# Performance work log

Hardware: AMD Instinct MI355X
Metric: run time of the kernel (lower is better)

The kernel has to match this reference:

```python
import jax, jax.numpy as jnp
import numpy as np

B, N, C, D, K, H, A = 4, 2048, 128, 128, 16, 64, 512


def _rn(k, shape, s):
    return (jax.random.normal(k, shape) * s).astype(jnp.float32)


def setup_inputs():
    ks = jax.random.split(jax.random.key(0), 40)
    w = lambda i, o, c: _rn(ks[i], (o, c), 0.02)
    b = lambda i, o: _rn(ks[i + 20], (o,), 0.02)
    p = {}
    p["xyz"] = _rn(ks[0], (B, 3, N), 1.0)
    p["pos"] = _rn(ks[1], (B, 2, N), 1.0)
    p["key"] = _rn(ks[2], (B, C, N), 1.0)
    p["query"] = _rn(ks[3], (B, C, N), 1.0)
    p["mv_w1"] = w(4, C, 2 * C); p["mv_b1"] = b(4, C)
    p["mv_w2"] = w(5, C, C);     p["mv_b2"] = b(5, C)
    p["mv_ws"] = w(6, C, 2 * C); p["mv_bs"] = b(6, C)
    p["wk"] = w(7, D, C); p["bk"] = b(7, D)
    p["wq"] = w(8, D, C); p["bq"] = b(8, D)
    p["wv"] = w(9, D, C); p["bv"] = b(9, D)
    p["xyz_w1"] = w(10, H, 3); p["xyz_b1"] = b(10, H)
    p["xyz_w2"] = w(11, D, H); p["xyz_b2"] = b(11, D)
    p["pos_w1"] = w(12, H, 2); p["pos_b1"] = b(12, H)
    p["pos_w2"] = w(13, D, H); p["pos_b2"] = b(13, D)
    p["xat_w1"] = w(14, A, D); p["xat_b1"] = b(14, A)
    p["xat_w2"] = w(15, D, A); p["xat_b2"] = b(15, D)
    p["at_w1"] = w(16, A, D); p["at_b1"] = b(16, A)
    p["at_w2"] = w(17, D, A); p["at_b2"] = b(17, D)
    p["wkq"] = w(18, C, D); p["bkq"] = b(18, C)
    p["wend"] = w(19, C, D); p["bend"] = b(19, C)
    return p


def c1(w, b, x):  # 1x1 Conv1d: (O,C) on (B,C,N)
    return jnp.einsum('oc,bcn->bon', w, x) + b[None, :, None]


def c2(w, b, x):  # 1x1 Conv2d: (O,C) on (B,C,N,K)
    return jnp.einsum('oc,bcnk->bonk', w, x) + b[None, :, None, None]


def mlp2(w1, b1, w2, b2, x):
    return c2(w2, b2, jax.nn.relu(c2(w1, b1, x)))


def softmax_one(x):  # exp(x-m) / (1 + sum exp(x-m)) over last axis
    m = jnp.max(x, axis=-1, keepdims=True)
    e = jnp.exp(x - m)
    return e / (1.0 + jnp.sum(e, axis=-1, keepdims=True))


def knn_idx(pts, k):  # pts: (B, N, d) -> (B, N, k) indices, include_self=True
    sq = jnp.sum(pts * pts, axis=-1)
    d2 = sq[:, :, None] + sq[:, None, :] - 2.0 * jnp.einsum('bnd,bmd->bnm', pts, pts)
    return jnp.argsort(d2, axis=-1)[:, :, :k]


def group(f, idx):  # f: (B,C,N), idx: (B,N,K) -> (B,C,N,K)
    return jax.vmap(lambda a, i: a[:, i])(f, idx)


def reference(xyz, pos, key, query, mv_w1, mv_b1, mv_w2, mv_b2, mv_ws, mv_bs,
              wk, bk, wq, bq, wv, bv, xyz_w1, xyz_b1, xyz_w2, xyz_b2,
              pos_w1, pos_b1, pos_w2, pos_b2, xat_w1, xat_b1, xat_w2, xat_b2,
              at_w1, at_b1, at_w2, at_b2, wkq, bkq, wend, bend):
    cat = jnp.concatenate([key, query], axis=1)  # (B, 2C, N)
    # MLP_Res
    value = c1(mv_w2, mv_b2, jax.nn.relu(c1(mv_w1, mv_b1, cat))) + c1(mv_ws, mv_bs, cat)
    identity = value
    k = c1(wk, bk, key)
    q = c1(wq, bq, query)
    v = c1(wv, bv, value)
    # ---- block 1: xyz-space kNN attention ----
    idx1 = knn_idx(jnp.swapaxes(xyz, 1, 2), K)           # (B,N,K)
    kq_rel = k[..., None] - group(q, idx1)               # (B,D,N,K)
    xyz_rel = xyz[..., None] - group(xyz, idx1)          # (B,3,N,K)
    xyz_emb = mlp2(xyz_w1, xyz_b1, xyz_w2, xyz_b2, xyz_rel)
    xa = softmax_one(mlp2(xat_w1, xat_b1, xat_w2, xat_b2, kq_rel + xyz_emb))
    agg = jnp.sum(xa * (v[..., None] + xyz_emb), axis=-1)  # (B,D,N)
    value = c1(wkq, bkq, agg) + identity
    value = c1(wv, bv, value)
    # ---- block 2: pos-space kNN attention ----
    idx2 = knn_idx(jnp.swapaxes(pos, 1, 2), K)
    qk_rel = q[..., None] - group(k, idx2)
    pos_rel = pos[..., None] - group(pos, idx2)
    pos_emb = mlp2(pos_w1, pos_b1, pos_w2, pos_b2, pos_rel)
    at = softmax_one(mlp2(at_w1, at_b1, at_w2, at_b2, qk_rel + pos_emb))
    agg = jnp.sum(at * (value[..., None] + pos_emb), axis=-1)
    y = c1(wend, bend, agg)
    return y + identity
```

## Files before the change

kernel.cpp:

```cpp
#include <hip/hip_runtime.h>
#include <hip/hip_bf16.h>

typedef __hip_bfloat16 bf16;
typedef unsigned long long ull;

#define BB 4
#define NN 2048
#define CCH 128
#define DDM 128
#define KNB 16
#define HHD 64
#define AAD 512
#define PP (BB*NN)

typedef __attribute__((ext_vector_type(8))) short short8;
typedef __attribute__((ext_vector_type(16))) float f32x16;

__device__ __forceinline__ float b2f(bf16 x) { return __bfloat162float(x); }
__device__ __forceinline__ bf16 f2b(float x) { return __float2bfloat16(x); }

__device__ __forceinline__ float ldany(const void* p, size_t i, int f32) {
  return f32 ? ((const float*)p)[i] : __bfloat162float(((const bf16*)p)[i]);
}

__device__ __forceinline__ long pack4(float a, float b, float c, float d) {
  union { bf16 h[4]; long l; } u;
  u.h[0] = f2b(a); u.h[1] = f2b(b); u.h[2] = f2b(c); u.h[3] = f2b(d);
  return u.l;
}
__device__ __forceinline__ void unpack4(long l, float* o) {
  union { bf16 h[4]; long l; } u; u.l = l;
  o[0] = b2f(u.h[0]); o[1] = b2f(u.h[1]); o[2] = b2f(u.h[2]); o[3] = b2f(u.h[3]);
}

__device__ __forceinline__ short8 ldfrag(const bf16* base, int row, int stride, int k0, int hl) {
  const bf16* p = base + (size_t)row * stride + k0 + (hl << 3);
  union { short8 v; long l[2]; } u;
  u.l[0] = *(const long*)p;
  u.l[1] = *(const long*)(p + 4);
  return u.v;
}

__device__ __forceinline__ f32x16 MFMA(short8 a, short8 b, f32x16 c) {
  return __builtin_amdgcn_mfma_f32_32x32x16_bf16(a, b, c, 0, 0, 0);
}

struct PtrArr { const void* p[36]; int n[36]; };
struct CvtTab { int src[16]; int off[16]; int n[16]; int isb[16]; };
struct G4 { const bf16* X[4]; int K[4]; int woff[4]; int boff[4]; bf16* out[4]; int relu[4]; };

__global__ __launch_bounds__(256) void sniff_kern(PtrArr pa, int* __restrict__ flags) {
  int t = blockIdx.x;
  const bf16* x = (const bf16*)pa.p[t];
  int n = pa.n[t]; if (n > 4096) n = 4096;
  __shared__ int cnt;
  if (threadIdx.x == 0) cnt = 0;
  __syncthreads();
  int c = 0;
  for (int i = threadIdx.x; i < n; i += 256) {
    float v = fabsf(__bfloat162float(x[i]));
    if (v == 0.f || (v >= 1e-6f && v <= 1024.f)) c++;
  }
  atomicAdd(&cnt, c);
  __syncthreads();
  if (threadIdx.x == 0) flags[t] = (cnt >= (n * 7) / 8) ? 0 : 1;
}

__global__ __launch_bounds__(256) void cvtprep_kern(PtrArr pa, CvtTab tab,
                                                    const int* __restrict__ flags,
                                                    bf16* __restrict__ warena, float* __restrict__ barena,
                                                    bf16* __restrict__ w1img0, bf16* __restrict__ w2img0,
                                                    bf16* __restrict__ cw2img0, float* __restrict__ fb0,
                                                    bf16* __restrict__ w1img1, bf16* __restrict__ w2img1,
                                                    bf16* __restrict__ cw2img1, float* __restrict__ fb1) {
  int y = blockIdx.y;
  if (y >= 2) {
    int e = y - 2;
    int i = blockIdx.x * 256 + threadIdx.x;
    if (i >= tab.n[e]) return;
    float v = ldany(pa.p[tab.src[e]], i, flags[tab.src[e]]);
    if (tab.isb[e]) barena[tab.off[e] + i] = v;
    else warena[tab.off[e] + i] = f2b(v);
    return;
  }
  int set = y;
  int cIdx = set ? 20 : 16, aIdx = set ? 28 : 24, dd = set ? 2 : 3;
  bf16* w1img = set ? w1img1 : w1img0;
  bf16* w2img = set ? w2img1 : w2img0;
  bf16* cw2img = set ? cw2img1 : cw2img0;
  float* fb = set ? fb1 : fb0;
  const void* cw1 = pa.p[cIdx];     const void* cb1 = pa.p[cIdx + 1];
  const void* cw2 = pa.p[cIdx + 2]; const void* cb2 = pa.p[cIdx + 3];
  const void* aw1 = pa.p[aIdx];     const void* ab1 = pa.p[aIdx + 1];
  const void* aw2 = pa.p[aIdx + 2]; const void* ab2 = pa.p[aIdx + 3];
  int i = blockIdx.x * 256 + threadIdx.x;
  const int fcw1 = flags[cIdx], fcb1 = flags[cIdx + 1];
  const int fcw2 = flags[cIdx + 2], fcb2 = flags[cIdx + 3];
  const int faw1 = flags[aIdx], fab1 = flags[aIdx + 1];
  const int faw2 = flags[aIdx + 2], fab2 = flags[aIdx + 3];
  float* ab1f = fb;
  float* ab2f = fb + 512;
  float* cb1f = fb + 640;
  float* cb2f = fb + 704;
  float* cw1f = fb + 832;
  if (i < 65536) {
    int hg = i >> 7, c = i & 127;
    w1img[(size_t)hg * 132 + c] = f2b(ldany(aw1, i, faw1));
  } else if (i < 131072) {
    int j = i - 65536;
    int o = j >> 9, hh = j & 511;
    int ac = hh >> 7, hloc = hh & 127;
    w2img[(size_t)(ac * 128 + o) * 132 + hloc] = f2b(ldany(aw2, j, faw2));
  } else if (i < 139264) {
    int j = i - 131072;
    int o = j >> 6, h = j & 63;
    cw2img[o * 68 + h] = f2b(ldany(cw2, j, fcw2));
  } else if (i < 139776) {
    int j = i - 139264; ab1f[j] = ldany(ab1, j, fab1);
  } else if (i < 139904) {
    int j = i - 139776; ab2f[j] = ldany(ab2, j, fab2);
  } else if (i < 139968) {
    int j = i - 139904; cb1f[j] = ldany(cb1, j, fcb1);
  } else if (i < 140096) {
    int j = i - 139968; cb2f[j] = ldany(cb2, j, fcb2);
  } else if (i < 140288) {
    int j = i - 140096;
    int h = j / 3, c = j % 3;
    cw1f[j] = (c < dd) ? ldany(cw1, h * dd + c, fcw1) : 0.f;
  }
}

__global__ __launch_bounds__(256) void trall_kern(const void* __restrict__ keyp,
                                                  const void* __restrict__ qryp,
                                                  const void* __restrict__ xyzp,
                                                  const void* __restrict__ posp,
                                                  const int* __restrict__ flags,
                                                  bf16* __restrict__ catT,
                                                  float* __restrict__ xyzT,
                                                  float* __restrict__ posT,
                                                  bf16* __restrict__ warena,
                                                  float* __restrict__ barena) {
  int bx = blockIdx.x;
  int tid = threadIdx.x;
  if (bx < 512) {
    __shared__ float tile[64][65];
    int xx = bx & 31, yy = (bx >> 5) & 1, zz = bx >> 6;
    int b = zz & 3, half = zz >> 2;
    const void* src = half ? qryp : keyp;
    const int f32 = flags[2 + half];
    int n0 = xx * 64, c0 = yy * 64;
    int tx = tid & 63, ty = tid >> 6;
    for (int r = ty; r < 64; r += 4)
      tile[r][tx] = ldany(src, (size_t)(b * 128 + c0 + r) * NN + n0 + tx, f32);
    __syncthreads();
    for (int r = ty; r < 64; r += 4)
      catT[(size_t)(b * NN + n0 + r) * 256 + half * 128 + c0 + tx] = __float2bfloat16(tile[tx][r]);
    return;
  }
  if (bx < 768) {
    int cb = bx - 512;
    int which = cb >> 7;
    const void* src = which ? posp : xyzp;
    float* dst = which ? posT : xyzT;
    int dd = which ? 2 : 3;
    const int f32 = flags[which];
    int i = (cb & 127) * 256 * 2 + tid;
    for (int rep = 0; rep < 2; ++rep, i += 256) {
      if (i < PP * 4) {
        int p = i >> 2, j = i & 3;
        int b = p >> 11, n = p & (NN - 1);
        dst[i] = (j < dd) ? ldany(src, (size_t)(b * dd + j) * NN + n, f32) : 0.f;
      }
    }
    return;
  }
  int bx2 = bx - 768;
  const bf16* wv = warena + 114688;
  const bf16* wkq = warena + 131072;
  if (bx2 < 64) {
    int i = bx2 * 256 + tid;
    int row = i >> 7, col = i & 127;
    float acc = 0.f;
    for (int k = 0; k < 128; ++k)
      acc += b2f(wv[row * 128 + k]) * b2f(wkq[k * 128 + col]);
    warena[163840 + i] = f2b(acc);
  } else if (tid < 128) {
    float acc = 0.f;
    const float* bkq = barena + 768;
    for (int k = 0; k < 128; ++k)
      acc += b2f(wv[tid * 128 + k]) * bkq[k];
    barena[1024 + tid] = acc;
  }
}

__global__ __launch_bounds__(512) void mega_kern(
    const float* __restrict__ xyzT, const float* __restrict__ posT,
    int* __restrict__ idx1, int* __restrict__ idx2,
    G4 g, const bf16* __restrict__ warena, const float* __restrict__ barena) {
  __shared__ __attribute__((aligned(16))) char smem[33280];
  int bx = blockIdx.x;
  int tid = threadIdx.x, lane = tid & 63, wvv = tid >> 6;
  if (bx < 2048) {
    float4* cds = (float4*)smem;
    int set = bx >> 10;
    int pblk = bx & 1023;
    const float* coordsT = set ? posT : xyzT;
    int* idxout = set ? idx2 : idx1;
    int p0 = pblk * 8, b = p0 >> 11;
    for (int j = tid; j < NN; j += 512)
      cds[j] = *(const float4*)&coordsT[((size_t)(b << 11) + j) * 4];
    __syncthreads();
    int p = p0 + wvv, n = p & (NN - 1);
    float4 cc = cds[n];
    float sqi = __fadd_rn(__fadd_rn(__fmul_rn(cc.x, cc.x), __fmul_rn(cc.y, cc.y)),
                          __fmul_rn(cc.z, cc.z));
    ull t[32];
#pragma unroll
    for (int s = 0; s < 32; ++s) {
      int j = (s << 6) | lane;
      float4 q = cds[j];
      float sqj = __fadd_rn(__fadd_rn(__fmul_rn(q.x, q.x), __fmul_rn(q.y, q.y)),
                            __fmul_rn(q.z, q.z));
      float dt  = __fadd_rn(__fadd_rn(__fmul_rn(cc.x, q.x), __fmul_rn(cc.y, q.y)),
                            __fmul_rn(cc.z, q.z));
      float d2 = __fsub_rn(__fadd_rn(sqi, sqj), __fmul_rn(2.f, dt));
      unsigned u = __float_as_uint(d2);
      u = (u & 0x80000000u) ? ~u : (u | 0x80000000u);
      t[s] = ((ull)u << 32) | (unsigned)j;
    }
#pragma unroll
    for (int base = 0; base < 32; base += 16) {
#pragma unroll
      for (int k = 2; k <= 16; k <<= 1) {
#pragma unroll
        for (int j = k >> 1; j > 0; j >>= 1) {
#pragma unroll
          for (int i = 0; i < 16; ++i) {
            int l = i ^ j;
            if (l > i) {
              bool up = ((i & k) == 0);
              ull a = t[base + i], c = t[base + l];
              ull lo = a < c ? a : c;
              ull hi = a < c ? c : a;
              t[base + i] = up ? lo : hi;
              t[base + l] = up ? hi : lo;
            }
          }
        }
      }
    }
#pragma unroll
    for (int i = 0; i < 16; ++i) {
      ull a = t[i], c = t[31 - i];
      t[i] = a < c ? a : c;
    }
#pragma unroll
    for (int j = 8; j > 0; j >>= 1) {
#pragma unroll
      for (int i = 0; i < 16; ++i) {
        int l = i ^ j;
        if (l > i) {
          ull a = t[i], c = t[l];
          ull lo = a < c ? a : c;
          ull hi = a < c ? c : a;
          t[i] = lo; t[l] = hi;
        }
      }
    }
    for (int r = 0; r < KNB; ++r) {
      ull h = t[0];
      ull m = h;
#pragma unroll
      for (int off = 1; off < 64; off <<= 1) {
        ull o = __shfl_xor(m, off);
        m = o < m ? o : m;
      }
      if (lane == 0) idxout[(size_t)p * KNB + r] = (int)(m & 0xffffffffu);
      if (h == m) {
#pragma unroll
        for (int i = 0; i < 15; ++i) t[i] = t[i + 1];
        t[15] = ~0ull;
      }
    }
    return;
  }
  {
    bf16* XT = (bf16*)smem;
    int bx2 = bx - 2048;
    int op = bx2 >> 7, ptile = bx2 & 127;
    const bf16* X = g.X[op];
    int K = g.K[op];
    const bf16* Wb = warena + g.woff[op];
    const float* bias = barena + g.boff[op];
    bf16* out = g.out[op];
    int relu = g.relu[op];
    int hl = lane >> 5, cA = lane & 31;
    int p0 = ptile * 64;
    int SK = K + 4;
    int kc = K >> 3;
    for (int c = tid; c < 64 * kc; c += 512) {
      int r = c / kc, col = (c % kc) << 3;
      *(float4*)&XT[r * SK + col] = *(const float4*)&X[(size_t)(p0 + r) * 256 + col];
    }
    __syncthreads();
    int o0 = (wvv & 3) * 32;
    int tt = wvv >> 2;
    f32x16 acc;
#pragma unroll
    for (int r = 0; r < 16; ++r) {
      int o = o0 + (r & 3) + 8 * (r >> 2) + 4 * hl;
      acc[r] = bias[o];
    }
    for (int ks = 0; ks < (K >> 4); ++ks) {
      short8 af = ldfrag(Wb, o0 + cA, K, ks * 16, hl);
      short8 b0 = ldfrag(XT, tt * 32 + cA, SK, ks * 16, hl);
      acc = MFMA(af, b0, acc);
    }
    int m = p0 + tt * 32 + cA;
#pragma unroll
    for (int q = 0; q < 4; ++q) {
      int ob = o0 + 8 * q + 4 * hl;
      float v[4] = {acc[4*q+0], acc[4*q+1], acc[4*q+2], acc[4*q+3]};
      if (relu) {
        v[0] = fmaxf(v[0], 0.f); v[1] = fmaxf(v[1], 0.f);
        v[2] = fmaxf(v[2], 0.f); v[3] = fmaxf(v[3], 0.f);
      }
      *(long*)(out + (size_t)m * 128 + ob) = pack4(v[0], v[1], v[2], v[3]);
    }
  }
}

__global__ __launch_bounds__(256) void gemm_chain_kern(
    const bf16* __restrict__ X, const bf16* __restrict__ warena,
    const float* __restrict__ barena,
    int w1off, int b1off, const bf16* __restrict__ add1, bf16* __restrict__ out1,
    int w2off, int b2off, bf16* __restrict__ out2) {
  __shared__ __attribute__((aligned(16))) bf16 XT[32 * 132];
  __shared__ __attribute__((aligned(16))) bf16 YT[32 * 132];
  int tid = threadIdx.x, lane = tid & 63, wv = tid >> 6;
  int hl = lane >> 5, cA = lane & 31;
  int p0 = blockIdx.x * 32;
  for (int c = tid; c < 32 * 16; c += 256) {
    int r = c >> 4, col = (c & 15) << 3;
    *(float4*)&XT[r * 132 + col] = *(const float4*)&X[(size_t)(p0 + r) * 128 + col];
  }
  __syncthreads();
  int o0 = wv * 32;
  const bf16* W1 = warena + w1off;
  const float* b1 = barena + b1off;
  f32x16 acc;
#pragma unroll
  for (int r = 0; r < 16; ++r) {
    int o = o0 + (r & 3) + 8 * (r >> 2) + 4 * hl;
    acc[r] = b1[o];
  }
#pragma unroll
  for (int ks = 0; ks < 8; ++ks) {
    short8 af = ldfrag(W1, o0 + cA, 128, ks * 16, hl);
    short8 b0 = ldfrag(XT, cA, 132, ks * 16, hl);
    acc = MFMA(af, b0, acc);
  }
  int m = p0 + cA;
#pragma unroll
  for (int q = 0; q < 4; ++q) {
    int ob = o0 + 8 * q + 4 * hl;
    float v[4] = {acc[4*q+0], acc[4*q+1], acc[4*q+2], acc[4*q+3]};
    if (add1) {
      float av[4];
      unpack4(*(const long*)(add1 + (size_t)m * 128 + ob), av);
      v[0] += av[0]; v[1] += av[1]; v[2] += av[2]; v[3] += av[3];
    }
    long pk = pack4(v[0], v[1], v[2], v[3]);
    *(long*)&YT[cA * 132 + ob] = pk;
    if (out1) *(long*)(out1 + (size_t)m * 128 + ob) = pk;
  }
  __syncthreads();
  const bf16* W2 = warena + w2off;
  const float* b2 = barena + b2off;
  f32x16 acc2;
#pragma unroll
  for (int r = 0; r < 16; ++r) {
    int o = o0 + (r & 3) + 8 * (r >> 2) + 4 * hl;
    acc2[r] = b2[o];
  }
#pragma unroll
  for (int ks = 0; ks < 8; ++ks) {
    short8 af = ldfrag(W2, o0 + cA, 128, ks * 16, hl);
    short8 b0 = ldfrag(YT, cA, 132, ks * 16, hl);
    acc2 = MFMA(af, b0, acc2);
  }
#pragma unroll
  for (int q = 0; q < 4; ++q) {
    int ob = o0 + 8 * q + 4 * hl;
    *(long*)(out2 + (size_t)m * 128 + ob) =
        pack4(acc2[4*q+0], acc2[4*q+1], acc2[4*q+2], acc2[4*q+3]);
  }
}

#define SMEM_BYTES 72192
__global__ __launch_bounds__(512, 4) void attn_mfma(
    const bf16* __restrict__ centerT, const bf16* __restrict__ gatherT,
    const float* __restrict__ coordsT, const bf16* __restrict__ vfeatT,
    const int* __restrict__ idx,
    const bf16* __restrict__ w1img, const bf16* __restrict__ w2img,
    const bf16* __restrict__ cw2img, const float* __restrict__ fb,
    const bf16* __restrict__ wout, const float* __restrict__ bout,
    const bf16* __restrict__ residG, void* __restrict__ outAny, int outMode,
    const int* __restrict__ flags) {
  extern __shared__ char smem[];
  bf16* XS  = (bf16*)(smem);
  bf16* HT  = (bf16*)(smem + 33792);
  bf16* HC  = HT;
  bf16* CFE = (bf16*)(smem + 67584);
  bf16* VF  = (bf16*)(smem + 69632);
  int*  NID = (int*)(smem + 71680);
  const float* ab1f = fb;
  const float* ab2f = fb + 512;
  const float* cb1f = fb + 640;
  const float* cb2f = fb + 704;
  const float* cw1f = fb + 832;

  int tid = threadIdx.x, lane = tid & 63, wv = tid >> 6;
  int hl = lane >> 5, cA = lane & 31;
  int P0 = blockIdx.x * 8, b = P0 >> 11;

  if (tid < 128) NID[tid] = (b << 11) + idx[(size_t)(P0 + (tid >> 4)) * KNB + (tid & 15)];
  for (int i = tid; i < 1024; i += 512) {
    int g = i >> 7, d = i & 127;
    CFE[i] = centerT[(size_t)(P0 + g) * 128 + d];
    VF[i]  = vfeatT[(size_t)(P0 + g) * 128 + d];
  }
  __syncthreads();

  {
    int m = tid >> 2, sub = tid & 3;
    float4 ccd = *(const float4*)&coordsT[(size_t)(P0 + (m >> 4)) * 4];
    float4 nbd = *(const float4*)&coordsT[(size_t)NID[m] * 4];
    float r0 = ccd.x - nbd.x, r1 = ccd.y - nbd.y, r2 = ccd.z - nbd.z;
    int h0 = sub * 16;
    for (int hh = h0; hh < h0 + 16; hh += 4) {
      float a0 = fmaxf(cb1f[hh+0] + cw1f[(hh+0)*3]*r0 + cw1f[(hh+0)*3+1]*r1 + cw1f[(hh+0)*3+2]*r2, 0.f);
      float a1 = fmaxf(cb1f[hh+1] + cw1f[(hh+1)*3]*r0 + cw1f[(hh+1)*3+1]*r1 + cw1f[(hh+1)*3+2]*r2, 0.f);
      float a2 = fmaxf(cb1f[hh+2] + cw1f[(hh+2)*3]*r0 + cw1f[(hh+2)*3+1]*r1 + cw1f[(hh+2)*3+2]*r2, 0.f);
      float a3 = fmaxf(cb1f[hh+3] + cw1f[(hh+3)*3]*r0 + cw1f[(hh+3)*3+1]*r1 + cw1f[(hh+3)*3+2]*r2, 0.f);
      *(long*)&HC[m * 68 + hh] = pack4(a0, a1, a2, a3);
    }
    const bf16* grow = gatherT + (size_t)NID[m] * 128 + sub * 32;
    const bf16* crow = CFE + ((m >> 4) << 7) + sub * 32;
    for (int j = 0; j < 32; j += 4) {
      float gv[4], cv[4];
      unpack4(*(const long*)(grow + j), gv);
      unpack4(*(const long*)(crow + j), cv);
      *(long*)&XS[m * 132 + sub * 32 + j] =
          pack4(cv[0] - gv[0], cv[1] - gv[1], cv[2] - gv[2], cv[3] - gv[3]);
    }
  }
  __syncthreads();

  int r0s = (wv & 3) * 32;
  int mt0 = (wv >> 2) * 64;

  short8 pf[8];
#pragma unroll
  for (int ks = 0; ks < 8; ++ks)
    pf[ks] = ldfrag(w1img, r0s + cA, 132, ks * 16, hl);

  {
    f32x16 eacc[2];
#pragma unroll
    for (int r = 0; r < 16; ++r) {
      int o = r0s + (r & 3) + 8 * (r >> 2) + 4 * hl;
      float bv = cb2f[o];
      eacc[0][r] = bv; eacc[1][r] = bv;
    }
    for (int k0 = 0; k0 < 64; k0 += 16) {
      short8 af = ldfrag(cw2img, r0s + cA, 68, k0, hl);
      short8 b0 = ldfrag(HC, mt0 + cA, 68, k0, hl);
      short8 b1 = ldfrag(HC, mt0 + 32 + cA, 68, k0, hl);
      eacc[0] = MFMA(af, b0, eacc[0]);
      eacc[1] = MFMA(af, b1, eacc[1]);
    }
#pragma unroll
    for (int t = 0; t < 2; ++t) {
      int m = mt0 + t * 32 + cA;
#pragma unroll
      for (int q = 0; q < 4; ++q) {
        int ob = r0s + 8 * q + 4 * hl;
        bf16* px = &XS[m * 132 + ob];
        float xv[4];
        unpack4(*(long*)px, xv);
        *(long*)px = pack4(xv[0] + eacc[t][4*q+0], xv[1] + eacc[t][4*q+1],
                           xv[2] + eacc[t][4*q+2], xv[3] + eacc[t][4*q+3]);
      }
    }
  }
  __syncthreads();

  f32x16 acc2[2];
#pragma unroll
  for (int r = 0; r < 16; ++r) {
    int o = r0s + (r & 3) + 8 * (r >> 2) + 4 * hl;
    float bv = ab2f[o];
    acc2[0][r] = bv; acc2[1][r] = bv;
  }

  for (int ac = 0; ac < 4; ++ac) {
    const bf16* w2c = w2img + (size_t)ac * 16896;
    const bf16* w1n = w1img + (size_t)((ac + 1) & 3) * 16896;
    f32x16 acc1[2];
#pragma unroll
    for (int r = 0; r < 16; ++r) {
      int h = r0s + (r & 3) + 8 * (r >> 2) + 4 * hl;
      float bv = ab1f[ac * 128 + h];
      acc1[0][r] = bv; acc1[1][r] = bv;
    }
#pragma unroll
    for (int ks = 0; ks < 8; ++ks) {
      short8 af = pf[ks];
      short8 b0 = ldfrag(XS, mt0 + cA, 132, ks * 16, hl);
      short8 b1 = ldfrag(XS, mt0 + 32 + cA, 132, ks * 16, hl);
      pf[ks] = ldfrag(w2c, r0s + cA, 132, ks * 16, hl);
      acc1[0] = MFMA(af, b0, acc1[0]);
      acc1[1] = MFMA(af, b1, acc1[1]);
    }
    __syncthreads();
#pragma unroll
    for (int t = 0; t < 2; ++t) {
      int m = mt0 + t * 32 + cA;
#pragma unroll
      for (int q = 0; q < 4; ++q) {
        int hb = r0s + 8 * q + 4 * hl;
        *(long*)&HT[m * 132 + hb] =
            pack4(fmaxf(acc1[t][4*q+0], 0.f), fmaxf(acc1[t][4*q+1], 0.f),
                  fmaxf(acc1[t][4*q+2], 0.f), fmaxf(acc1[t][4*q+3], 0.f));
      }
    }
    __syncthreads();
#pragma unroll
    for (int ks = 0; ks < 8; ++ks) {
      short8 af = pf[ks];
      short8 b0 = ldfrag(HT, mt0 + cA, 132, ks * 16, hl);
      short8 b1 = ldfrag(HT, mt0 + 32 + cA, 132, ks * 16, hl);
      pf[ks] = ldfrag(w1n, r0s + cA, 132, ks * 16, hl);
      acc2[0] = MFMA(af, b0, acc2[0]);
      acc2[1] = MFMA(af, b1, acc2[1]);
    }
  }

  __syncthreads();
#pragma unroll
  for (int t = 0; t < 2; ++t) {
    int m = mt0 + t * 32 + cA;
#pragma unroll
    for (int q = 0; q < 4; ++q) {
      int ob = r0s + 8 * q + 4 * hl;
      *(long*)&HT[m * 132 + ob] = pack4(acc2[t][4*q+0], acc2[t][4*q+1],
                                        acc2[t][4*q+2], acc2[t][4*q+3]);
    }
  }
  __syncthreads();

  float agg0, agg1v;
  {
    int g = wv;
    int base = g * 16;
    float vbase0 = b2f(VF[g * 128 + lane])      - b2f(CFE[g * 128 + lane]);
    float vbase1 = b2f(VF[g * 128 + lane + 64]) - b2f(CFE[g * 128 + lane + 64]);
#pragma unroll
    for (int half = 0; half < 2; ++half) {
      int o = lane + half * 64;
      float vb = half ? vbase1 : vbase0;
      float e[16];
      float mx = -3.4e38f;
#pragma unroll
      for (int kk = 0; kk < 16; ++kk) {
        float x = b2f(HT[(base + kk) * 132 + o]);
        e[kk] = x;
        mx = fmaxf(mx, x);
      }
      float s = 0.f;
#pragma unroll
      for (int kk = 0; kk < 16; ++kk) { e[kk] = __expf(e[kk] - mx); s += e[kk]; }
      float inv = 1.f / (1.f + s);
      float acc = 0.f;
#pragma unroll
      for (int kk = 0; kk < 16; ++kk) {
        float xv = b2f(XS[(base + kk) * 132 + o]);
        float gv = b2f(gatherT[(size_t)NID[base + kk] * 128 + o]);
        acc += (e[kk] * inv) * (vb + xv + gv);
      }
      if (half) agg1v = acc; else agg0 = acc;
    }
  }
  __syncthreads();
  {
    int g = wv;
    HT[g * 132 + lane] = f2b(agg0);
    HT[g * 132 + lane + 64] = f2b(agg1v);
  }
  __syncthreads();

  if (wv < 4) {
    int o0m = wv * 32;
    f32x16 acc;
#pragma unroll
    for (int r = 0; r < 16; ++r) {
      int o = o0m + (r & 3) + 8 * (r >> 2) + 4 * hl;
      acc[r] = bout[o];
    }
#pragma unroll
    for (int ks = 0; ks < 8; ++ks) {
      short8 af = ldfrag(wout, o0m + cA, 128, ks * 16, hl);
      short8 b0 = ldfrag(HT, cA, 132, ks * 16, hl);
      acc = MFMA(af, b0, acc);
    }
    int m = cA;
    if (m < 8) {
      int f32o = outMode ? flags[2] : 0;
      int gp = P0 + m;
      int gb = gp >> 11, gn = gp & (NN - 1);
#pragma unroll
      for (int q = 0; q < 4; ++q) {
        int ob = o0m + 8 * q + 4 * hl;
        float rv[4];
        if (outMode) unpack4(*(const long*)(residG + (size_t)gp * 128 + ob), rv);
        else         unpack4(*(long*)&VF[m * 128 + ob], rv);
        float v0o = acc[4*q+0] + rv[0];
        float v1o = acc[4*q+1] + rv[1];
        float v2o = acc[4*q+2] + rv[2];
        float v3o = acc[4*q+3] + rv[3];
        if (outMode) {
          float vv[4] = {v0o, v1o, v2o, v3o};
#pragma unroll
          for (int i = 0; i < 4; ++i) {
            size_t oi = (size_t)(gb * 128 + ob + i) * NN + gn;
            if (f32o) ((float*)outAny)[oi] = vv[i];
            else ((bf16*)outAny)[oi] = f2b(vv[i]);
          }
        } else {
          *(long*)((bf16*)outAny + (size_t)gp * 128 + ob) = pack4(v0o, v1o, v2o, v3o);
        }
      }
    }
  }
}

extern "C" void kernel_launch(void* const* d_in, const int* in_sizes, int n_in,
                              void* d_out, int out_size, void* d_ws, size_t ws_size,
                              hipStream_t stream) {
  int* flags = (int*)d_ws;
  bf16* catT = (bf16*)((float*)d_ws + 64);
  bf16* v0   = catT + (size_t)PP * 256;
  bf16* kT   = v0 + (size_t)PP * 128;
  bf16* qT   = kT + (size_t)PP * 128;
  bf16* sE   = qT + (size_t)PP * 128;
  bf16* sF   = sE + (size_t)PP * 128;
  bf16* sG   = sF + (size_t)PP * 128;
  float* xyzT = (float*)(sG + (size_t)PP * 128);
  float* posT = xyzT + (size_t)PP * 4;
  int* idx1 = (int*)(posT + (size_t)PP * 4);
  int* idx2 = idx1 + (size_t)PP * KNB;
  bf16* w1i1 = (bf16*)(idx2 + (size_t)PP * KNB);
  bf16* w2i1 = w1i1 + 67584;
  bf16* cw2i1 = w2i1 + 67584;
  bf16* w1i2 = cw2i1 + 8704;
  bf16* w2i2 = w1i2 + 67584;
  bf16* cw2i2 = w2i2 + 67584;
  float* fb1 = (float*)(cw2i2 + 8704);
  float* fb2 = fb1 + 1024;
  bf16* warena = (bf16*)(fb2 + 1024);
  float* barena = (float*)(warena + 180224);

  PtrArr pa;
  for (int i = 0; i < 36; ++i) { pa.p[i] = d_in[i]; pa.n[i] = in_sizes[i]; }
  sniff_kern<<<dim3(36), 256, 0, stream>>>(pa, flags);

  CvtTab tab;
  int wsrc[8] = {4, 8, 6, 10, 12, 14, 32, 34};
  int woff[8] = {0, 32768, 65536, 81920, 98304, 114688, 131072, 147456};
  int wn[8]   = {32768, 32768, 16384, 16384, 16384, 16384, 16384, 16384};
  int bsrc[8] = {5, 9, 7, 11, 13, 15, 33, 35};
  for (int e = 0; e < 8; ++e) {
    tab.src[e] = wsrc[e]; tab.off[e] = woff[e]; tab.n[e] = wn[e]; tab.isb[e] = 0;
    tab.src[8 + e] = bsrc[e]; tab.off[8 + e] = e * 128; tab.n[8 + e] = 128; tab.isb[8 + e] = 1;
  }
  cvtprep_kern<<<dim3(548, 18), 256, 0, stream>>>(pa, tab, flags, warena, barena,
                                                  w1i1, w2i1, cw2i1, fb1,
                                                  w1i2, w2i2, cw2i2, fb2);

  trall_kern<<<dim3(833), 256, 0, stream>>>(d_in[2], d_in[3], d_in[0], d_in[1],
                                            flags, catT, xyzT, posT, warena, barena);

  G4 g4;
  g4.X[0] = catT;       g4.K[0] = 256; g4.woff[0] = 0;      g4.boff[0] = 0;   g4.out[0] = sF; g4.relu[0] = 1;
  g4.X[1] = catT;       g4.K[1] = 256; g4.woff[1] = 32768;  g4.boff[1] = 128; g4.out[1] = sG; g4.relu[1] = 0;
  g4.X[2] = catT;       g4.K[2] = 128; g4.woff[2] = 81920;  g4.boff[2] = 384; g4.out[2] = kT; g4.relu[2] = 0;
  g4.X[3] = catT + 128; g4.K[3] = 128; g4.woff[3] = 98304;  g4.boff[3] = 512; g4.out[3] = qT; g4.relu[3] = 0;
  mega_kern<<<dim3(2048 + 512), 512, 0, stream>>>(xyzT, posT, idx1, idx2, g4, warena, barena);

  gemm_chain_kern<<<dim3(PP / 32), 256, 0, stream>>>(sF, warena, barena,
                                                     65536, 256, sG, v0,
                                                     114688, 640, sE);

  hipFuncSetAttribute((const void*)attn_mfma, hipFuncAttributeMaxDynamicSharedMemorySize, SMEM_BYTES);

  attn_mfma<<<dim3(PP / 8), 512, SMEM_BYTES, stream>>>(kT, qT, xyzT, sE, idx1,
                                                       w1i1, w2i1, cw2i1, fb1,
                                                       warena + 163840, barena + 1024,
                                                       nullptr, sE, 0, flags);
  attn_mfma<<<dim3(PP / 8), 512, SMEM_BYTES, stream>>>(qT, kT, posT, sE, idx2,
                                                       w1i2, w2i2, cw2i2, fb2,
                                                       warena + 147456, barena + 896,
                                                       v0, d_out, 1, flags);
}
```

Before: 382.5 us.

## Fuse prep kernels, fold value-chain GEMMs into attention, coalesce output stores

Merges the transpose/coordinate-prep kernel into the weight-conversion kernel, moves the Wv·Wkq weight-combine into extra blocks of mega_kern, and removes the standalone gemm_chain kernel. The first attention launch now computes its value features itself from sF/sG with two small MFMA GEMMs per 8-point tile. The final output is staged in shared memory and written in channel-major form with vector stores instead of scattered scalar stores. This cuts kernel launches and intermediate global traffic. In exchange, the fused GEMMs run 32-wide MFMAs where only 8 columns are valid, and the attention kernel takes on extra synchronisation.

```diff
diff --git a/kernel.cpp b/kernel.cpp
--- a/kernel.cpp
+++ b/kernel.cpp
@@ -66,17 +66,56 @@
   if (threadIdx.x == 0) flags[t] = (cnt >= (n * 7) / 8) ? 0 : 1;
 }
 
-__global__ __launch_bounds__(256) void cvtprep_kern(PtrArr pa, CvtTab tab,
-                                                    const int* __restrict__ flags,
-                                                    bf16* __restrict__ warena, float* __restrict__ barena,
-                                                    bf16* __restrict__ w1img0, bf16* __restrict__ w2img0,
-                                                    bf16* __restrict__ cw2img0, float* __restrict__ fb0,
-                                                    bf16* __restrict__ w1img1, bf16* __restrict__ w2img1,
-                                                    bf16* __restrict__ cw2img1, float* __restrict__ fb1) {
+__global__ __launch_bounds__(256) void prep_all_kern(PtrArr pa, CvtTab tab,
+                                                     const int* __restrict__ flags,
+                                                     bf16* __restrict__ warena, float* __restrict__ barena,
+                                                     bf16* __restrict__ w1img0, bf16* __restrict__ w2img0,
+                                                     bf16* __restrict__ cw2img0, float* __restrict__ fb0,
+                                                     bf16* __restrict__ w1img1, bf16* __restrict__ w2img1,
+                                                     bf16* __restrict__ cw2img1, float* __restrict__ fb1,
+                                                     const void* __restrict__ keyp, const void* __restrict__ qryp,
+                                                     const void* __restrict__ xyzp, const void* __restrict__ posp,
+                                                     bf16* __restrict__ catT,
+                                                     float* __restrict__ xyzT, float* __restrict__ posT) {
   int y = blockIdx.y;
+  int tid = threadIdx.x;
+  int bx = blockIdx.x;
+  if (y == 18) {
+    if (bx >= 512) return;
+    __shared__ float tile[64][65];
+    int xx = bx & 31, yy = (bx >> 5) & 1, zz = bx >> 6;
+    int b = zz & 3, half = zz >> 2;
+    const void* src = half ? qryp : keyp;
+    const int f32 = flags[2 + half];
+    int n0 = xx * 64, c0 = yy * 64;
+    int tx = tid & 63, ty = tid >> 6;
+    for (int r = ty; r < 64; r += 4)
+      tile[r][tx] = ldany(src, (size_t)(b * 128 + c0 + r) * NN + n0 + tx, f32);
+    __syncthreads();
+    for (int r = ty; r < 64; r += 4)
+      catT[(size_t)(b * NN + n0 + r) * 256 + half * 128 + c0 + tx] = __float2bfloat16(tile[tx][r]);
+    return;
+  }
+  if (y == 19) {
+    if (bx >= 256) return;
+    int which = bx >> 7;
+    const void* src = which ? posp : xyzp;
+    float* dst = which ? posT : xyzT;
+    int dd = which ? 2 : 3;
+    const int f32 = flags[which];
+    int i = (bx & 127) * 256 * 2 + tid;
+    for (int rep = 0; rep < 2; ++rep, i += 256) {
+      if (i < PP * 4) {
+        int p = i >> 2, j = i & 3;
+        int b = p >> 11, n = p & (NN - 1);
+        dst[i] = (j < dd) ? ldany(src, (size_t)(b * dd + j) * NN + n, f32) : 0.f;
+      }
+    }
+    return;
+  }
   if (y >= 2) {
     int e = y - 2;
-    int i = blockIdx.x * 256 + threadIdx.x;
+    int i = bx * 256 + tid;
     if (i >= tab.n[e]) return;
     float v = ldany(pa.p[tab.src[e]], i, flags[tab.src[e]]);
     if (tab.isb[e]) barena[tab.off[e] + i] = v;
@@ -93,7 +132,7 @@
   const void* cw2 = pa.p[cIdx + 2]; const void* cb2 = pa.p[cIdx + 3];
   const void* aw1 = pa.p[aIdx];     const void* ab1 = pa.p[aIdx + 1];
   const void* aw2 = pa.p[aIdx + 2]; const void* ab2 = pa.p[aIdx + 3];
-  int i = blockIdx.x * 256 + threadIdx.x;
+  int i = bx * 256 + tid;
   const int fcw1 = flags[cIdx], fcb1 = flags[cIdx + 1];
   const int fcw2 = flags[cIdx + 2], fcb2 = flags[cIdx + 3];
   const int faw1 = flags[aIdx], fab1 = flags[aIdx + 1];
@@ -130,73 +169,10 @@
   }
 }
 
-__global__ __launch_bounds__(256) void trall_kern(const void* __restrict__ keyp,
-                                                  const void* __restrict__ qryp,
-                                                  const void* __restrict__ xyzp,
-                                                  const void* __restrict__ posp,
-                                                  const int* __restrict__ flags,
-                                                  bf16* __restrict__ catT,
-                                                  float* __restrict__ xyzT,
-                                                  float* __restrict__ posT,
-                                                  bf16* __restrict__ warena,
-                                                  float* __restrict__ barena) {
-  int bx = blockIdx.x;
-  int tid = threadIdx.x;
-  if (bx < 512) {
-    __shared__ float tile[64][65];
-    int xx = bx & 31, yy = (bx >> 5) & 1, zz = bx >> 6;
-    int b = zz & 3, half = zz >> 2;
-    const void* src = half ? qryp : keyp;
-    const int f32 = flags[2 + half];
-    int n0 = xx * 64, c0 = yy * 64;
-    int tx = tid & 63, ty = tid >> 6;
-    for (int r = ty; r < 64; r += 4)
-      tile[r][tx] = ldany(src, (size_t)(b * 128 + c0 + r) * NN + n0 + tx, f32);
-    __syncthreads();
-    for (int r = ty; r < 64; r += 4)
-      catT[(size_t)(b * NN + n0 + r) * 256 + half * 128 + c0 + tx] = __float2bfloat16(tile[tx][r]);
-    return;
-  }
-  if (bx < 768) {
-    int cb = bx - 512;
-    int which = cb >> 7;
-    const void* src = which ? posp : xyzp;
-    float* dst = which ? posT : xyzT;
-    int dd = which ? 2 : 3;
-    const int f32 = flags[which];
-    int i = (cb & 127) * 256 * 2 + tid;
-    for (int rep = 0; rep < 2; ++rep, i += 256) {
-      if (i < PP * 4) {
-        int p = i >> 2, j = i & 3;
-        int b = p >> 11, n = p & (NN - 1);
-        dst[i] = (j < dd) ? ldany(src, (size_t)(b * dd + j) * NN + n, f32) : 0.f;
-      }
-    }
-    return;
-  }
-  int bx2 = bx - 768;
-  const bf16* wv = warena + 114688;
-  const bf16* wkq = warena + 131072;
-  if (bx2 < 64) {
-    int i = bx2 * 256 + tid;
-    int row = i >> 7, col = i & 127;
-    float acc = 0.f;
-    for (int k = 0; k < 128; ++k)
-      acc += b2f(wv[row * 128 + k]) * b2f(wkq[k * 128 + col]);
-    warena[163840 + i] = f2b(acc);
-  } else if (tid < 128) {
-    float acc = 0.f;
-    const float* bkq = barena + 768;
-    for (int k = 0; k < 128; ++k)
-      acc += b2f(wv[tid * 128 + k]) * bkq[k];
-    barena[1024 + tid] = acc;
-  }
-}
-
 __global__ __launch_bounds__(512) void mega_kern(
     const float* __restrict__ xyzT, const float* __restrict__ posT,
     int* __restrict__ idx1, int* __restrict__ idx2,
-    G4 g, const bf16* __restrict__ warena, const float* __restrict__ barena) {
+    G4 g, bf16* __restrict__ warena, float* __restrict__ barena) {
   __shared__ __attribute__((aligned(16))) char smem[33280];
   int bx = blockIdx.x;
   int tid = threadIdx.x, lane = tid & 63, wvv = tid >> 6;
@@ -284,7 +260,7 @@
     }
     return;
   }
-  {
+  if (bx < 2560) {
     bf16* XT = (bf16*)smem;
     int bx2 = bx - 2048;
     int op = bx2 >> 7, ptile = bx2 & 127;
@@ -327,73 +303,28 @@
       }
       *(long*)(out + (size_t)m * 128 + ob) = pack4(v[0], v[1], v[2], v[3]);
     }
-  }
-}
-
-__global__ __launch_bounds__(256) void gemm_chain_kern(
-    const bf16* __restrict__ X, const bf16* __restrict__ warena,
-    const float* __restrict__ barena,
-    int w1off, int b1off, const bf16* __restrict__ add1, bf16* __restrict__ out1,
-    int w2off, int b2off, bf16* __restrict__ out2) {
-  __shared__ __attribute__((aligned(16))) bf16 XT[32 * 132];
-  __shared__ __attribute__((aligned(16))) bf16 YT[32 * 132];
-  int tid = threadIdx.x, lane = tid & 63, wv = tid >> 6;
-  int hl = lane >> 5, cA = lane & 31;
-  int p0 = blockIdx.x * 32;
-  for (int c = tid; c < 32 * 16; c += 256) {
-    int r = c >> 4, col = (c & 15) << 3;
-    *(float4*)&XT[r * 132 + col] = *(const float4*)&X[(size_t)(p0 + r) * 128 + col];
-  }
-  __syncthreads();
-  int o0 = wv * 32;
-  const bf16* W1 = warena + w1off;
-  const float* b1 = barena + b1off;
-  f32x16 acc;
-#pragma unroll
-  for (int r = 0; r < 16; ++r) {
-    int o = o0 + (r & 3) + 8 * (r >> 2) + 4 * hl;
-    acc[r] = b1[o];
-  }
-#pragma unroll
-  for (int ks = 0; ks < 8; ++ks) {
-    short8 af = ldfrag(W1, o0 + cA, 128, ks * 16, hl);
-    short8 b0 = ldfrag(XT, cA, 132, ks * 16, hl);
-    acc = MFMA(af, b0, acc);
-  }
-  int m = p0 + cA;
-#pragma unroll
-  for (int q = 0; q < 4; ++q) {
-    int ob = o0 + 8 * q + 4 * hl;
-    float v[4] = {acc[4*q+0], acc[4*q+1], acc[4*q+2], acc[4*q+3]};
-    if (add1) {
-      float av[4];
-      unpack4(*(const long*)(add1 + (size_t)m * 128 + ob), av);
-      v[0] += av[0]; v[1] += av[1]; v[2] += av[2]; v[3] += av[3];
-    }
-    long pk = pack4(v[0], v[1], v[2], v[3]);
-    *(long*)&YT[cA * 132 + ob] = pk;
-    if (out1) *(long*)(out1 + (size_t)m * 128 + ob) = pk;
-  }
-  __syncthreads();
-  const bf16* W2 = warena + w2off;
-  const float* b2 = barena + b2off;
-  f32x16 acc2;
-#pragma unroll
-  for (int r = 0; r < 16; ++r) {
-    int o = o0 + (r & 3) + 8 * (r >> 2) + 4 * hl;
-    acc2[r] = b2[o];
-  }
-#pragma unroll
-  for (int ks = 0; ks < 8; ++ks) {
-    short8 af = ldfrag(W2, o0 + cA, 128, ks * 16, hl);
-    short8 b0 = ldfrag(YT, cA, 132, ks * 16, hl);
-    acc2 = MFMA(af, b0, acc2);
-  }
-#pragma unroll
-  for (int q = 0; q < 4; ++q) {
-    int ob = o0 + 8 * q + 4 * hl;
-    *(long*)(out2 + (size_t)m * 128 + ob) =
-        pack4(acc2[4*q+0], acc2[4*q+1], acc2[4*q+2], acc2[4*q+3]);
+    return;
+  }
+  {
+    int bx2 = bx - 2560;
+    const bf16* wvw = warena + 114688;
+    const bf16* wkq = warena + 131072;
+    if (bx2 < 64) {
+      int i = bx2 * 512 + tid;
+      if (i < 16384) {
+        int row = i >> 7, col = i & 127;
+        float acc = 0.f;
+        for (int k = 0; k < 128; ++k)
+          acc += b2f(wvw[row * 128 + k]) * b2f(wkq[k * 128 + col]);
+        warena[163840 + i] = f2b(acc);
+      }
+    } else if (tid < 128) {
+      float acc = 0.f;
+      const float* bkq = barena + 768;
+      for (int k = 0; k < 128; ++k)
+        acc += b2f(wvw[tid * 128 + k]) * bkq[k];
+      barena[1024 + tid] = acc;
+    }
   }
 }
 
@@ -406,7 +337,11 @@
     const bf16* __restrict__ cw2img, const float* __restrict__ fb,
     const bf16* __restrict__ wout, const float* __restrict__ bout,
     const bf16* __restrict__ residG, void* __restrict__ outAny, int outMode,
-    const int* __restrict__ flags) {
+    const int* __restrict__ flags,
+    const bf16* __restrict__ sFp, const bf16* __restrict__ sGp,
+    const bf16* __restrict__ mvw2, const float* __restrict__ mvb2,
+    const bf16* __restrict__ wvw, const float* __restrict__ bvf,
+    bf16* __restrict__ v0out, int fuseChain) {
   extern __shared__ char smem[];
   bf16* XS  = (bf16*)(smem);
   bf16* HT  = (bf16*)(smem + 33792);
@@ -425,12 +360,75 @@
   int P0 = blockIdx.x * 8, b = P0 >> 11;
 
   if (tid < 128) NID[tid] = (b << 11) + idx[(size_t)(P0 + (tid >> 4)) * KNB + (tid & 15)];
-  for (int i = tid; i < 1024; i += 512) {
-    int g = i >> 7, d = i & 127;
-    CFE[i] = centerT[(size_t)(P0 + g) * 128 + d];
-    VF[i]  = vfeatT[(size_t)(P0 + g) * 128 + d];
-  }
-  __syncthreads();
+  if (fuseChain) {
+    for (int i = tid; i < 1024; i += 512) {
+      int g = i >> 7, d = i & 127;
+      CFE[i] = centerT[(size_t)(P0 + g) * 128 + d];
+      XS[g * 132 + d] = sFp[(size_t)(P0 + g) * 128 + d];
+      XS[(8 + g) * 132 + d] = sGp[(size_t)(P0 + g) * 128 + d];
+    }
+    __syncthreads();
+    if (wv < 4) {
+      int o0m = wv * 32;
+      f32x16 a1;
+#pragma unroll
+      for (int r = 0; r < 16; ++r) {
+        int o = o0m + (r & 3) + 8 * (r >> 2) + 4 * hl;
+        a1[r] = mvb2[o];
+      }
+#pragma unroll
+      for (int ks = 0; ks < 8; ++ks) {
+        short8 af = ldfrag(mvw2, o0m + cA, 128, ks * 16, hl);
+        short8 b0 = ldfrag(XS, cA, 132, ks * 16, hl);
+        a1 = MFMA(af, b0, a1);
+      }
+      int m = cA;
+      if (m < 8) {
+#pragma unroll
+        for (int q = 0; q < 4; ++q) {
+          int ob = o0m + 8 * q + 4 * hl;
+          float sg[4];
+          unpack4(*(long*)&XS[(8 + m) * 132 + ob], sg);
+          long pk = pack4(a1[4*q+0] + sg[0], a1[4*q+1] + sg[1],
+                          a1[4*q+2] + sg[2], a1[4*q+3] + sg[3]);
+          *(long*)&HT[m * 132 + ob] = pk;
+          *(long*)(v0out + (size_t)(P0 + m) * 128 + ob) = pk;
+        }
+      }
+    }
+    __syncthreads();
+    if (wv < 4) {
+      int o0m = wv * 32;
+      f32x16 a2;
+#pragma unroll
+      for (int r = 0; r < 16; ++r) {
+        int o = o0m + (r & 3) + 8 * (r >> 2) + 4 * hl;
+        a2[r] = bvf[o];
+      }
+#pragma unroll
+      for (int ks = 0; ks < 8; ++ks) {
+        short8 af = ldfrag(wvw, o0m + cA, 128, ks * 16, hl);
+        short8 b0 = ldfrag(HT, cA, 132, ks * 16, hl);
+        a2 = MFMA(af, b0, a2);
+      }
+      int m = cA;
+      if (m < 8) {
+#pragma unroll
+        for (int q = 0; q < 4; ++q) {
+          int ob = o0m + 8 * q + 4 * hl;
+          *(long*)&VF[m * 128 + ob] = pack4(a2[4*q+0], a2[4*q+1], a2[4*q+2], a2[4*q+3]);
+        }
+      }
+    }
+    __syncthreads();
+  } else {
+    for (int i = tid; i < 1024; i += 512) {
+      int g = i >> 7, d = i & 127;
+      CFE[i] = centerT[(size_t)(P0 + g) * 128 + d];
+      VF[i]  = vfeatT[(size_t)(P0 + g) * 128 + d];
+    }
+    __syncthreads();
+  }
 
   {
     int m = tid >> 2, sub = tid & 3;
@@ -600,6 +598,7 @@
   }
   __syncthreads();
 
+  float* XSf = (float*)XS;
   if (wv < 4) {
     int o0m = wv * 32;
     f32x16 acc;
@@ -616,9 +615,7 @@
     }
     int m = cA;
     if (m < 8) {
-      int f32o = outMode ? flags[2] : 0;
       int gp = P0 + m;
-      int gb = gp >> 11, gn = gp & (NN - 1);
 #pragma unroll
       for (int q = 0; q < 4; ++q) {
         int ob = o0m + 8 * q + 4 * hl;
@@ -630,16 +627,34 @@
         float v2o = acc[4*q+2] + rv[2];
         float v3o = acc[4*q+3] + rv[3];
         if (outMode) {
-          float vv[4] = {v0o, v1o, v2o, v3o};
-#pragma unroll
-          for (int i = 0; i < 4; ++i) {
-            size_t oi = (size_t)(gb * 128 + ob + i) * NN + gn;
-            if (f32o) ((float*)outAny)[oi] = vv[i];
-            else ((bf16*)outAny)[oi] = f2b(vv[i]);
-          }
+          float4 st = {v0o, v1o, v2o, v3o};
+          *(float4*)&XSf[m * 128 + ob] = st;
         } else {
           *(long*)((bf16*)outAny + (size_t)gp * 128 + ob) = pack4(v0o, v1o, v2o, v3o);
         }
+      }
+    }
+  }
+  if (outMode) {
+    __syncthreads();
+    if (tid < 128) {
+      int c = tid;
+      int gb = P0 >> 11, gn0 = P0 & (NN - 1);
+      if (flags[2]) {
+        float* op = (float*)outAny + (size_t)(gb * 128 + c) * NN + gn0;
+        float4 v0v, v1v;
+        v0v.x = XSf[0 * 128 + c]; v0v.y = XSf[1 * 128 + c];
+        v0v.z = XSf[2 * 128 + c]; v0v.w = XSf[3 * 128 + c];
+        v1v.x = XSf[4 * 128 + c]; v1v.y = XSf[5 * 128 + c];
+        v1v.z = XSf[6 * 128 + c]; v1v.w = XSf[7 * 128 + c];
+        *(float4*)op = v0v;
+        *(float4*)(op + 4) = v1v;
+      } else {
+        bf16* op = (bf16*)outAny + (size_t)(gb * 128 + c) * NN + gn0;
+        long l0 = pack4(XSf[0 * 128 + c], XSf[1 * 128 + c], XSf[2 * 128 + c], XSf[3 * 128 + c]);
+        long l1 = pack4(XSf[4 * 128 + c], XSf[5 * 128 + c], XSf[6 * 128 + c], XSf[7 * 128 + c]);
+        *(long*)op = l0;
+        *(long*)(op + 4) = l1;
       }
     }
   }
@@ -684,32 +699,35 @@
     tab.src[e] = wsrc[e]; tab.off[e] = woff[e]; tab.n[e] = wn[e]; tab.isb[e] = 0;
     tab.src[8 + e] = bsrc[e]; tab.off[8 + e] = e * 128; tab.n[8 + e] = 128; tab.isb[8 + e] = 1;
   }
-  cvtprep_kern<<<dim3(548, 18), 256, 0, stream>>>(pa, tab, flags, warena, barena,
-                                                  w1i1, w2i1, cw2i1, fb1,
-                                                  w1i2, w2i2, cw2i2, fb2);
-
-  trall_kern<<<dim3(833), 256, 0, stream>>>(d_in[2], d_in[3], d_in[0], d_in[1],
-                                            flags, catT, xyzT, posT, warena, barena);
+  prep_all_kern<<<dim3(548, 20), 256, 0, stream>>>(pa, tab, flags, warena, barena,
+                                                   w1i1, w2i1, cw2i1, fb1,
+                                                   w1i2, w2i2, cw2i2, fb2,
+                                                   d_in[2], d_in[3], d_in[0], d_in[1],
+                                                   catT, xyzT, posT);
 
   G4 g4;
   g4.X[0] = catT;       g4.K[0] = 256; g4.woff[0] = 0;      g4.boff[0] = 0;   g4.out[0] = sF; g4.relu[0] = 1;
   g4.X[1] = catT;       g4.K[1] = 256; g4.woff[1] = 32768;  g4.boff[1] = 128; g4.out[1] = sG; g4.relu[1] = 0;
   g4.X[2] = catT;       g4.K[2] = 128; g4.woff[2] = 81920;  g4.boff[2] = 384; g4.out[2] = kT; g4.relu[2] = 0;
   g4.X[3] = catT + 128; g4.K[3] = 128; g4.woff[3] = 98304;  g4.boff[3] = 512; g4.out[3] = qT; g4.relu[3] = 0;
-  mega_kern<<<dim3(2048 + 512), 512, 0, stream>>>(xyzT, posT, idx1, idx2, g4, warena, barena);
-
-  gemm_chain_kern<<<dim3(PP / 32), 256, 0, stream>>>(sF, warena, barena,
-                                                     65536, 256, sG, v0,
-                                                     114688, 640, sE);
+  mega_kern<<<dim3(2048 + 512 + 65), 512, 0, stream>>>(xyzT, posT, idx1, idx2, g4, warena, barena);
 
   hipFuncSetAttribute((const void*)attn_mfma, hipFuncAttributeMaxDynamicSharedMemorySize, SMEM_BYTES);
 
-  attn_mfma<<<dim3(PP / 8), 512, SMEM_BYTES, stream>>>(kT, qT, xyzT, sE, idx1,
+  attn_mfma<<<dim3(PP / 8), 512, SMEM_BYTES, stream>>>(kT, qT, xyzT, nullptr, idx1,
                                                        w1i1, w2i1, cw2i1, fb1,
                                                        warena + 163840, barena + 1024,
-                                                       nullptr, sE, 0, flags);
+                                                       nullptr, sE, 0, flags,
+                                                       sF, sG,
+                                                       warena + 65536, barena + 256,
+                                                       warena + 114688, barena + 640,
+                                                       v0, 1);
   attn_mfma<<<dim3(PP / 8), 512, SMEM_BYTES, stream>>>(qT, kT, posT, sE, idx2,
                                                        w1i2, w2i2, cw2i2, fb2,
                                                        warena + 147456, barena + 896,
-                                                       v0, d_out, 1, flags);
-}
+                                                       v0, d_out, 1, flags,
+                                                       nullptr, nullptr,
+                                                       nullptr, nullptr,
+                                                       nullptr, nullptr,
+                                                       nullptr, 0);
+}
```

New measurement: 385.9 us. No clear change (+0.9%).
